# Optimization experiments

Hardware: AMD Instinct MI355X
Metric: run time of the kernel (lower is better)

Reference implementation:

```python
import jax, jax.numpy as jnp
import numpy as np

NUM_CLASSES = 91
COST_CLASS, COST_BBOX, COST_GIOU = 1.0, 5.0, 2.0
W_CE, W_BBOX, W_GIOU = 2.0, 2.5, 2.0
EOS_COEF = 0.1
B, Q, T = 64, 300, 25


def box_cxcywh_to_xyxy(x):
    cx, cy, w, h = x[..., 0], x[..., 1], x[..., 2], x[..., 3]
    return jnp.stack([cx - 0.5 * w, cy - 0.5 * h, cx + 0.5 * w, cy + 0.5 * h], axis=-1)


def giou_pairwise(b1, b2):
    # b1 [N,4], b2 [M,4] in xyxy -> [N,M]
    area1 = (b1[:, 2] - b1[:, 0]) * (b1[:, 3] - b1[:, 1])
    area2 = (b2[:, 2] - b2[:, 0]) * (b2[:, 3] - b2[:, 1])
    lt = jnp.maximum(b1[:, None, :2], b2[None, :, :2])
    rb = jnp.minimum(b1[:, None, 2:], b2[None, :, 2:])
    wh = jnp.clip(rb - lt, 0.0)
    inter = wh[..., 0] * wh[..., 1]
    union = area1[:, None] + area2[None, :] - inter
    iou = inter / union
    lti = jnp.minimum(b1[:, None, :2], b2[None, :, :2])
    rbi = jnp.maximum(b1[:, None, 2:], b2[None, :, 2:])
    whi = jnp.clip(rbi - lti, 0.0)
    areai = whi[..., 0] * whi[..., 1]
    return iou - (areai - union) / areai


def giou_elementwise(b1, b2):
    # b1,b2 [N,4] xyxy -> [N]
    area1 = (b1[:, 2] - b1[:, 0]) * (b1[:, 3] - b1[:, 1])
    area2 = (b2[:, 2] - b2[:, 0]) * (b2[:, 3] - b2[:, 1])
    lt = jnp.maximum(b1[:, :2], b2[:, :2])
    rb = jnp.minimum(b1[:, 2:], b2[:, 2:])
    wh = jnp.clip(rb - lt, 0.0)
    inter = wh[:, 0] * wh[:, 1]
    union = area1 + area2 - inter
    iou = inter / union
    lti = jnp.minimum(b1[:, :2], b2[:, :2])
    rbi = jnp.maximum(b1[:, 2:], b2[:, 2:])
    whi = jnp.clip(rbi - lti, 0.0)
    areai = whi[:, 0] * whi[:, 1]
    return iou - (areai - union) / areai


def _lsa(cost):
    # Jonker-Volgenant shortest augmenting path; same optimum as scipy linear_sum_assignment
    cost = np.asarray(cost, dtype=np.float64)
    transposed = cost.shape[0] > cost.shape[1]
    if transposed:
        cost = cost.T
    n, m = cost.shape  # n <= m
    u = np.zeros(n + 1)
    v = np.zeros(m + 1)
    p = np.zeros(m + 1, dtype=np.int64)
    way = np.zeros(m + 1, dtype=np.int64)
    for i in range(1, n + 1):
        p[0] = i
        j0 = 0
        minv = np.full(m + 1, np.inf)
        used = np.zeros(m + 1, dtype=bool)
        while True:
            used[j0] = True
            i0 = p[j0]
            cur = cost[i0 - 1, :] - u[i0] - v[1:]
            free = ~used[1:]
            better = free & (cur < minv[1:])
            minv[1:][better] = cur[better]
            way[1:][better] = j0
            masked = np.where(free, minv[1:], np.inf)
            j1 = int(np.argmin(masked)) + 1
            delta = minv[j1]
            u[p[used]] += delta
            v[used] -= delta
            minv[~used] -= delta
            j0 = j1
            if p[j0] == 0:
                break
        while j0:
            j1 = way[j0]
            p[j0] = p[j1]
            j0 = j1
    rows, cols = [], []
    for j in range(1, m + 1):
        if p[j] != 0:
            rows.append(p[j] - 1)
            cols.append(j - 1)
    rows = np.asarray(rows, dtype=np.int64)
    cols = np.asarray(cols, dtype=np.int64)
    if transposed:
        rows, cols = cols, rows
    order = np.argsort(rows)
    return rows[order], cols[order]


def _match(pred_logits, pred_boxes, tgt_labels, tgt_boxes):
    # builds the full cross-batch cost matrix exactly like the torch module, then
    # solves per-image rectangular assignment on the host (non-differentiable)
    log_prob = jax.nn.log_softmax(pred_logits.reshape(B * Q, NUM_CLASSES + 1), axis=-1)
    out_bbox = pred_boxes.reshape(B * Q, 4)
    tgt_ids = tgt_labels.reshape(B * T)
    tgt_bb = tgt_boxes.reshape(B * T, 4)
    cost_class = -log_prob[:, tgt_ids]                                        # [BQ, BT]
    cost_bbox = jnp.abs(out_bbox[:, None, :] - tgt_bb[None, :, :]).sum(-1)    # L1 cdist
    cost_giou = -giou_pairwise(box_cxcywh_to_xyxy(out_bbox), box_cxcywh_to_xyxy(tgt_bb))
    C = COST_BBOX * cost_bbox + COST_CLASS * cost_class + COST_GIOU * cost_giou
    Cn = np.asarray(jax.lax.stop_gradient(C.reshape(B, Q, B * T)))
    src = np.zeros((B, T), dtype=np.int64)
    tgt = np.zeros((B, T), dtype=np.int64)
    for b in range(B):
        r, c = _lsa(Cn[b, :, b * T:(b + 1) * T])
        src[b] = r
        tgt[b] = c
    batch_idx = jnp.repeat(jnp.arange(B), T)
    return batch_idx, jnp.asarray(src.reshape(-1)), jnp.asarray(tgt.reshape(-1))


def _losses(pred_logits, pred_boxes, tgt_labels, tgt_boxes, batch_idx, src_idx, tgt_idx):
    num_t = batch_idx.shape[0]
    matched_labels = tgt_labels[batch_idx, tgt_idx]
    target_classes = jnp.full((B, Q), NUM_CLASSES, dtype=jnp.int32)
    target_classes = target_classes.at[batch_idx, src_idx].set(matched_labels)
    empty_weight = jnp.ones(NUM_CLASSES + 1, dtype=pred_logits.dtype).at[-1].set(EOS_COEF)
    logp = jax.nn.log_softmax(pred_logits, axis=-1)
    nll = -jnp.take_along_axis(logp, target_classes[..., None], axis=-1)[..., 0]
    w = empty_weight[target_classes]
    loss_ce = (w * nll).sum() / w.sum()
    src_b = pred_boxes[batch_idx, src_idx]
    tgt_b = tgt_boxes[batch_idx, tgt_idx]
    loss_bbox = jnp.abs(src_b - tgt_b).sum() / num_t
    loss_giou = (1.0 - giou_elementwise(box_cxcywh_to_xyxy(src_b), box_cxcywh_to_xyxy(tgt_b))).sum() / num_t
    l_ce = W_CE * loss_ce
    l_bb = W_BBOX * loss_bbox
    l_gi = W_GIOU * loss_giou
    return jnp.stack([l_ce, l_bb, l_gi, l_ce + l_bb + l_gi])


def setup_inputs() -> dict:
    key = jax.random.key(0)
    k1, k2, k3, k4 = jax.random.split(key, 4)
    pred_logits = jax.random.normal(k1, (B, Q, NUM_CLASSES + 1), dtype=jnp.float32)
    pred_boxes = jax.random.uniform(k2, (B, Q, 4), dtype=jnp.float32, minval=0.05, maxval=0.95)
    tgt_labels = jax.random.randint(k3, (B, T), 0, NUM_CLASSES)
    tgt_boxes = jax.random.uniform(k4, (B, T, 4), dtype=jnp.float32, minval=0.05, maxval=0.95)
    return {"pred_logits": pred_logits, "pred_boxes": pred_boxes, "tgt_labels": tgt_labels, "tgt_boxes": tgt_boxes}


def reference(pred_logits, pred_boxes, tgt_labels, tgt_boxes):
    batch_idx, src_idx, tgt_idx = _match(pred_logits, pred_boxes, tgt_labels, tgt_boxes)
    # returns [loss_ce, loss_bbox, loss_giou, loss_total] (already weight-scaled)
    return _losses(pred_logits, pred_boxes, tgt_labels, tgt_boxes, batch_idx, src_idx, tgt_idx)
```

## Files before the change

kernel.cpp:

```cpp
#include <hip/hip_runtime.h>
#include <math.h>

constexpr int B_ = 64;
constexpr int Q_ = 300;
constexpr int T_ = 25;
constexpr int NCLS = 91;
constexpr int L_ = NCLS + 1;
constexpr float C_BB = 5.0f, C_GI = 2.0f;
constexpr float W_CE = 2.0f, W_BBOX = 2.5f, W_GIOU = 2.0f;
constexpr float EOS = 0.1f;
constexpr int K_ = 5;
constexpr int TPB = 256;

__device__ __forceinline__ unsigned long long ord64(double v) {
    long long bb = __double_as_longlong(v);
    return (bb < 0) ? ~(unsigned long long)bb
                    : ((unsigned long long)bb | 0x8000000000000000ULL);
}
__device__ __forceinline__ double unord64(unsigned long long u) {
    long long bb = (u & 0x8000000000000000ULL) ? (long long)(u & 0x7FFFFFFFFFFFFFFFULL)
                                               : (long long)~u;
    return __longlong_as_double(bb);
}
__device__ __forceinline__ unsigned long long pack14(double v, unsigned aux) {
    return (ord64(v) & ~16383ULL) | (unsigned long long)aux;
}
__device__ __forceinline__ unsigned long long pack9(double v, unsigned col) {
    return (ord64(v) & ~511ULL) | (unsigned long long)col;
}

template <int CTRL>
__device__ __forceinline__ unsigned long long dppb(unsigned long long b) {
    int lo = __builtin_amdgcn_update_dpp(0, (int)(unsigned)b, CTRL, 0xF, 0xF, true);
    int hi = __builtin_amdgcn_update_dpp(0, (int)(unsigned)(b >> 32), CTRL, 0xF, 0xF, true);
    return ((unsigned long long)(unsigned)hi << 32) | (unsigned)lo;
}
__device__ __forceinline__ unsigned long long swz16(unsigned long long b) {
    int lo = __builtin_amdgcn_ds_swizzle((int)(unsigned)b, 0x401F);
    int hi = __builtin_amdgcn_ds_swizzle((int)(unsigned)(b >> 32), 0x401F);
    return ((unsigned long long)(unsigned)hi << 32) | (unsigned)lo;
}

__device__ __forceinline__ unsigned long long wavemin(unsigned long long b) {
    { unsigned long long o = __shfl_xor(b, 32); if (o < b) b = o; }
    { unsigned long long o = swz16(b);      if (o < b) b = o; }
    { unsigned long long o = dppb<0x140>(b); if (o < b) b = o; }
    { unsigned long long o = dppb<0x141>(b); if (o < b) b = o; }
    { unsigned long long o = dppb<0x4E>(b);  if (o < b) b = o; }
    { unsigned long long o = dppb<0xB1>(b);  if (o < b) b = o; }
    return b;
}
__device__ __forceinline__ void red2(unsigned long long& k1, unsigned long long& k2,
                                     unsigned long long o1, unsigned long long o2) {
    unsigned long long n1 = o1 < k1 ? o1 : k1;
    unsigned long long ls = o1 < k1 ? k1 : o1;
    unsigned long long n2 = k2 < o2 ? k2 : o2;
    n2 = ls < n2 ? ls : n2;
    k1 = n1; k2 = n2;
}
__device__ __forceinline__ void wavemin2(unsigned long long& k1, unsigned long long& k2) {
    red2(k1, k2, __shfl_xor(k1, 32), __shfl_xor(k2, 32));
    red2(k1, k2, swz16(k1), swz16(k2));
    red2(k1, k2, dppb<0x140>(k1), dppb<0x140>(k2));
    red2(k1, k2, dppb<0x141>(k1), dppb<0x141>(k2));
    red2(k1, k2, dppb<0x4E>(k1),  dppb<0x4E>(k2));
    red2(k1, k2, dppb<0xB1>(k1),  dppb<0xB1>(k2));
}

__device__ __forceinline__ float giou_f(const float px[4], float parea,
                                        const float tx[4], float tarea) {
    float ltx = fmaxf(px[0], tx[0]), lty = fmaxf(px[1], tx[1]);
    float rbx = fminf(px[2], tx[2]), rby = fminf(px[3], tx[3]);
    float iw = fmaxf(rbx - ltx, 0.f), ih = fmaxf(rby - lty, 0.f);
    float inter = iw * ih;
    float uni = parea + tarea - inter;
    float iou = inter / uni;
    float lix = fminf(px[0], tx[0]), liy = fminf(px[1], tx[1]);
    float rix = fmaxf(px[2], tx[2]), riy = fmaxf(px[3], tx[3]);
    float aw = fmaxf(rix - lix, 0.f), ah = fmaxf(riy - liy, 0.f);
    float ai = aw * ah;
    return iou - (ai - uni) / ai;
}

__global__ __launch_bounds__(TPB) void fused_kernel(
        const float* __restrict__ logits,
        const float* __restrict__ pboxes,
        const int*   __restrict__ tlabels,
        const float* __restrict__ tboxes,
        double* __restrict__ partial) {
    const int b = blockIdx.x;
    const int tid = threadIdx.x;

    __shared__ float  costL[T_][Q_];
    __shared__ float  lseL[Q_];
    __shared__ int    pL[Q_ + 1];
    __shared__ int    wayL[Q_ + 1];
    __shared__ double uStage[32];
    __shared__ int    argcolL[T_];
    __shared__ float  m1L[T_];
    __shared__ double m2L[T_];
    __shared__ int    mqL[T_];
    __shared__ int    lblL[T_];
    __shared__ int    lblq[Q_];
    __shared__ float  tbL[T_][4];
    __shared__ float  txL[T_][4];
    __shared__ float  taL[T_];
    __shared__ double wsum[4][3];

    if (tid < T_) {
        lblL[tid] = tlabels[b * T_ + tid];
        mqL[tid] = 0;
        float c0 = tboxes[(size_t)(b * T_ + tid) * 4 + 0];
        float c1 = tboxes[(size_t)(b * T_ + tid) * 4 + 1];
        float c2 = tboxes[(size_t)(b * T_ + tid) * 4 + 2];
        float c3 = tboxes[(size_t)(b * T_ + tid) * 4 + 3];
        tbL[tid][0] = c0; tbL[tid][1] = c1; tbL[tid][2] = c2; tbL[tid][3] = c3;
        float x0 = c0 - 0.5f * c2, y0 = c1 - 0.5f * c3;
        float x1 = c0 + 0.5f * c2, y1 = c1 + 0.5f * c3;
        txL[tid][0] = x0; txL[tid][1] = y0; txL[tid][2] = x1; txL[tid][3] = y1;
        taL[tid] = (x1 - x0) * (y1 - y0);
    }
    for (int j = tid; j <= Q_; j += TPB) { pL[j] = 0; wayL[j] = 0; }
    for (int q = tid; q < Q_; q += TPB) lblq[q] = NCLS;
    __syncthreads();

    const float* lgb = logits + (size_t)b * Q_ * L_;
    const float* pbb = pboxes + (size_t)b * Q_ * 4;

    for (int q = tid; q < Q_; q += TPB) {
        const float4* lr4 = (const float4*)(lgb + (size_t)q * L_);
        float m0 = -INFINITY, m1 = -INFINITY, m2 = -INFINITY, m3 = -INFINITY;
        for (int c = 0; c < 23; ++c) {
            float4 v = lr4[c];
            m0 = fmaxf(m0, v.x); m1 = fmaxf(m1, v.y);
            m2 = fmaxf(m2, v.z); m3 = fmaxf(m3, v.w);
        }
        float mx = fmaxf(fmaxf(m0, m1), fmaxf(m2, m3));
        float s0 = 0.f, s1 = 0.f, s2 = 0.f, s3 = 0.f;
        for (int c = 0; c < 23; ++c) {
            float4 v = lr4[c];
            s0 += expf(v.x - mx); s1 += expf(v.y - mx);
            s2 += expf(v.z - mx); s3 += expf(v.w - mx);
        }
        float lz = mx + logf((s0 + s1) + (s2 + s3));
        lseL[q] = lz;

        float p0 = pbb[(size_t)q * 4 + 0], p1 = pbb[(size_t)q * 4 + 1];
        float p2 = pbb[(size_t)q * 4 + 2], p3 = pbb[(size_t)q * 4 + 3];
        float px[4] = { p0 - 0.5f * p2, p1 - 0.5f * p3, p0 + 0.5f * p2, p1 + 0.5f * p3 };
        float parea = (px[2] - px[0]) * (px[3] - px[1]);

#pragma unroll
        for (int t = 0; t < T_; ++t) {
            float cls = lz - lgb[(size_t)q * L_ + lblL[t]];
            float l1 = fabsf(p0 - tbL[t][0]) + fabsf(p1 - tbL[t][1]) +
                       fabsf(p2 - tbL[t][2]) + fabsf(p3 - tbL[t][3]);
            float tx[4] = { txL[t][0], txL[t][1], txL[t][2], txL[t][3] };
            float g = giou_f(px, parea, tx, taL[t]);
            costL[t][q] = C_BB * l1 + cls - C_GI * g;
        }
    }
    __syncthreads();

    {
        int w = tid >> 6, lane = tid & 63;
        for (int t = w; t < T_; t += 4) {
            unsigned long long k1 = ~0ULL, k2 = ~0ULL;
#pragma unroll
            for (int k = 0; k < K_; ++k) {
                int col = lane + 64 * k;
                if (col < Q_) {
                    unsigned long long kk = pack9((double)costL[t][col], (unsigned)col);
                    if (kk < k1) { k2 = k1; k1 = kk; }
                    else if (kk < k2) { k2 = kk; }
                }
            }
            wavemin2(k1, k2);
            if (lane == 0) {
                int jc = (int)(k1 & 511ULL);
                argcolL[t] = jc;
                m1L[t] = costL[t][jc];
                m2L[t] = unord64(k2 & ~511ULL);
            }
        }
    }
    __syncthreads();

    if (tid < 64) {
        bool isrow = (tid >= 1 && tid <= T_);
        int r0 = tid - 1;
        int myc = isrow ? argcolL[r0] : -1;
        bool winner = isrow;
        if (isrow) {
            for (int j = 0; j < r0; ++j)
                if (argcolL[j] == myc) winner = false;
        }
        int rowcol = (isrow && winner) ? myc + 1 : 0;
        unsigned long long mbal = __ballot(isrow && winner);
        unsigned int freemask = (~(unsigned int)(mbal >> 1)) & ((1u << T_) - 1);

        double ureg = 0.0;
        if (isrow) ureg = winner ? m2L[r0] : (double)m1L[r0];

        double v0[K_], minv[K_], stampv[K_];
        int pReg[K_];
        bool usedk[K_], validk[K_];
#pragma unroll
        for (int k = 0; k < K_; ++k) {
            int col = tid + 64 * k;
            validk[k] = col < Q_;
            v0[k] = 0.0; stampv[k] = 0.0; usedk[k] = false; minv[k] = INFINITY;
            pReg[k] = 0;
        }

        for (int t = 0; t < T_; ++t) {
            if ((mbal >> (t + 1)) & 1ULL) {
                int jc = argcolL[t];
                if (tid == (jc & 63)) {
                    int ki = jc >> 6;
                    double d = m2L[t] - (double)m1L[t];
                    if (d < 0.0) d = 0.0;
#pragma unroll
                    for (int k = 0; k < K_; ++k)
                        if (k == ki) { v0[k] -= d; pReg[k] = t + 1; }
                }
            }
        }

        for (int iter = 0; iter < 96 && freemask; ++iter) {
            int t = __builtin_ctz(freemask);
            freemask &= freemask - 1;
            const float* crow = &costL[t][0];
            unsigned long long k1 = ~0ULL, k2 = ~0ULL;
#pragma unroll
            for (int k = 0; k < K_; ++k) {
                if (validk[k]) {
                    int col = tid + 64 * k;
                    unsigned long long kk = pack9((double)crow[col] - v0[k], (unsigned)col);
                    if (kk < k1) { k2 = k1; k1 = kk; }
                    else if (kk < k2) { k2 = kk; }
                }
            }
            wavemin2(k1, k2);
            int j1 = (int)(k1 & 511ULL);
            double am1 = unord64(k1 & ~511ULL);
            double am2 = unord64(k2 & ~511ULL);
            unsigned long long bal = __ballot(rowcol == j1 + 1);
            int prev1 = bal ? __builtin_ctzll(bal) : 0;
            if (tid == (j1 & 63)) {
                int ki = j1 >> 6;
#pragma unroll
                for (int k = 0; k < K_; ++k)
                    if (k == ki) { v0[k] -= (am2 - am1); pReg[k] = t + 1; }
            }
            if (tid == t + 1) { ureg = am2; rowcol = j1 + 1; }
            if (prev1) {
                if (tid == prev1) rowcol = 0;
                freemask |= 1u << (prev1 - 1);
            }
        }

#pragma unroll
        for (int k = 0; k < K_; ++k)
            if (validk[k]) pL[tid + 1 + 64 * k] = pReg[k];

        for (int i = 1; i <= T_; ++i) {
            if (!((freemask >> (i - 1)) & 1u)) continue;
            if (tid == 0) pL[0] = i;
#pragma unroll
            for (int k = 0; k < K_; ++k) { minv[k] = INFINITY; usedk[k] = false; }
            double S = 0.0;
            int j0 = 0, i0 = i;
            double u0i0 = __shfl(ureg, i);

            for (int step = 0; step < 512; ++step) {
                double a = u0i0 - S;
                const float* crow = &costL[i0 - 1][0];
                unsigned long long bk = ~0ULL;
#pragma unroll
                for (int k = 0; k < K_; ++k) {
                    if (validk[k] && !usedk[k]) {
                        int col = tid + 64 * k;
                        double cur = (double)crow[col] - a - v0[k];
                        if (cur < minv[k]) { minv[k] = cur; wayL[col + 1] = j0; }
                        unsigned long long kk = pack14(
                            minv[k], ((unsigned)(col + 1) << 5) | (unsigned)pReg[k]);
                        if (kk < bk) bk = kk;
                    }
                }
                bk = wavemin(bk);
                int j1  = (int)((bk >> 5) & 511ULL);
                int i0n = (int)(bk & 31ULL);
                double Snew = unord64(bk & ~16383ULL);
                S = Snew;
                j0 = j1;
                if (i0n == 0) break;
                int owner = (j1 - 1) & 63, k1i = (j1 - 1) >> 6;
                if (tid == owner) {
#pragma unroll
                    for (int k = 0; k < K_; ++k)
                        if (k == k1i) { usedk[k] = true; stampv[k] = Snew; }
                }
                i0 = i0n;
                u0i0 = __shfl(ureg, i0);
            }

            if (tid <= T_) uStage[tid] = 0.0;
#pragma unroll
            for (int k = 0; k < K_; ++k) {
                if (validk[k] && usedk[k]) {
                    double d = S - stampv[k];
                    v0[k] -= d;
                    uStage[pReg[k]] = d;
                }
            }
            if (tid >= 1 && tid <= T_) ureg += uStage[tid];
            if (tid == i) ureg += S;
            if (tid == 0) {
                int jj = j0;
                while (jj) { int jn = wayL[jj]; pL[jj] = pL[jn]; jj = jn; }
            }
#pragma unroll
            for (int k = 0; k < K_; ++k)
                if (validk[k]) pReg[k] = pL[tid + 1 + 64 * k];
        }

#pragma unroll
        for (int k = 0; k < K_; ++k)
            if (validk[k] && pReg[k] > 0) mqL[pReg[k] - 1] = tid + 64 * k;
        if (tid < T_) lblq[mqL[tid]] = lblL[tid];
    }
    __syncthreads();

    double ce = 0.0, sb = 0.0, sg = 0.0;
    for (int q = tid; q < Q_; q += TPB) {
        int label = lblq[q];
        float nll = lseL[q] - lgb[(size_t)q * L_ + label];
        float w = (label == NCLS) ? EOS : 1.0f;
        ce += (double)(w * nll);
    }
    if (tid < T_) {
        int q = mqL[tid];
        float p0 = pbb[(size_t)q * 4 + 0], p1 = pbb[(size_t)q * 4 + 1];
        float p2 = pbb[(size_t)q * 4 + 2], p3 = pbb[(size_t)q * 4 + 3];
        sb = (double)(fabsf(p0 - tbL[tid][0]) + fabsf(p1 - tbL[tid][1]) +
                      fabsf(p2 - tbL[tid][2]) + fabsf(p3 - tbL[tid][3]));
        float px[4] = { p0 - 0.5f * p2, p1 - 0.5f * p3, p0 + 0.5f * p2, p1 + 0.5f * p3 };
        float parea = (px[2] - px[0]) * (px[3] - px[1]);
        float tx[4] = { txL[tid][0], txL[tid][1], txL[tid][2], txL[tid][3] };
        float g = giou_f(px, parea, tx, taL[tid]);
        sg = (double)(1.0f - g);
    }
#pragma unroll
    for (int off = 1; off < 64; off <<= 1) {
        ce += __shfl_xor(ce, off);
        sb += __shfl_xor(sb, off);
        sg += __shfl_xor(sg, off);
    }
    if ((tid & 63) == 0) {
        int w = tid >> 6;
        wsum[w][0] = ce; wsum[w][1] = sb; wsum[w][2] = sg;
    }
    __syncthreads();
    if (tid == 0) {
        double a0 = 0, a1 = 0, a2 = 0;
        for (int w = 0; w < 4; ++w) { a0 += wsum[w][0]; a1 += wsum[w][1]; a2 += wsum[w][2]; }
        partial[(size_t)b * 3 + 0] = a0;
        partial[(size_t)b * 3 + 1] = a1;
        partial[(size_t)b * 3 + 2] = a2;
    }
}

__global__ __launch_bounds__(64) void finalize_kernel(const double* __restrict__ partial,
                                                      float* __restrict__ out) {
    int tid = threadIdx.x;
    double a = partial[(size_t)tid * 3 + 0];
    double c = partial[(size_t)tid * 3 + 1];
    double g = partial[(size_t)tid * 3 + 2];
#pragma unroll
    for (int off = 1; off < 64; off <<= 1) {
        a += __shfl_xor(a, off);
        c += __shfl_xor(c, off);
        g += __shfl_xor(g, off);
    }
    if (tid == 0) {
        float lce = W_CE * (float)(a / 3360.0);
        float lbb = W_BBOX * (float)(c / 1600.0);
        float lgi = W_GIOU * (float)(g / 1600.0);
        out[0] = lce;
        out[1] = lbb;
        out[2] = lgi;
        out[3] = lce + lbb + lgi;
    }
}

extern "C" void kernel_launch(void* const* d_in, const int* in_sizes, int n_in,
                              void* d_out, int out_size, void* d_ws, size_t ws_size,
                              hipStream_t stream) {
    (void)in_sizes; (void)n_in; (void)out_size; (void)ws_size;
    const float* logits  = (const float*)d_in[0];
    const float* pboxes  = (const float*)d_in[1];
    const int*   tlabels = (const int*)d_in[2];
    const float* tboxes  = (const float*)d_in[3];
    float* out = (float*)d_out;
    double* partial = (double*)d_ws;

    fused_kernel<<<B_, TPB, 0, stream>>>(logits, pboxes, tlabels, tboxes, partial);
    finalize_kernel<<<1, 64, 0, stream>>>(partial, out);
}
```

Baseline: 39.99 us.

## Parallelize auction-style augmentation across four waves and fuse finalize via atomics

The single-wave serial augmentation phase becomes a multi-wave round loop. Each of the 4 waves bids for a different free row, and thread 0 resolves column conflicts and updates prices held in shared memory (vL, uL). The dual variables move from registers to shared memory so every wave can see them. The separate finalize kernel is removed: blocks accumulate with double atomics, and the last block, found with a counter, writes the output. A memset is added to zero the accumulator. The change trades per-round __syncthreads and serial resolution for fewer serial iterations, and it removes a kernel launch.

New measurement: 41.90 us. 1.05x slower.

```diff
diff --git a/kernel.cpp b/kernel.cpp
--- a/kernel.cpp
+++ b/kernel.cpp
@@ -87,18 +87,24 @@
         const float* __restrict__ pboxes,
         const int*   __restrict__ tlabels,
         const float* __restrict__ tboxes,
-        double* __restrict__ partial) {
+        double* acc,
+        float* out) {
     const int b = blockIdx.x;
     const int tid = threadIdx.x;
 
     __shared__ float  costL[T_][Q_];
     __shared__ float  lseL[Q_];
+    __shared__ double vL[Q_];
     __shared__ int    pL[Q_ + 1];
     __shared__ int    wayL[Q_ + 1];
-    __shared__ double uStage[32];
+    __shared__ double uL[T_ + 1];
     __shared__ int    argcolL[T_];
     __shared__ float  m1L[T_];
     __shared__ double m2L[T_];
+    __shared__ int    bidRowL[4];
+    __shared__ int    bidJL[4];
+    __shared__ double bidM1L[4], bidM2L[4];
+    __shared__ unsigned freemaskL;
     __shared__ int    mqL[T_];
     __shared__ int    lblL[T_];
     __shared__ int    lblq[Q_];
@@ -121,7 +127,7 @@
         taL[tid] = (x1 - x0) * (y1 - y0);
     }
     for (int j = tid; j <= Q_; j += TPB) { pL[j] = 0; wayL[j] = 0; }
-    for (int q = tid; q < Q_; q += TPB) lblq[q] = NCLS;
+    for (int q = tid; q < Q_; q += TPB) { lblq[q] = NCLS; vL[q] = 0.0; }
     __syncthreads();
 
     const float* lgb = logits + (size_t)b * Q_ * L_;
@@ -195,13 +201,76 @@
             for (int j = 0; j < r0; ++j)
                 if (argcolL[j] == myc) winner = false;
         }
-        int rowcol = (isrow && winner) ? myc + 1 : 0;
+        if (isrow) {
+            uL[tid] = winner ? m2L[r0] : (double)m1L[r0];
+            if (winner) {
+                pL[myc + 1] = tid;
+                double d = m2L[r0] - (double)m1L[r0];
+                if (d < 0.0) d = 0.0;
+                vL[myc] = -d;
+            }
+        }
         unsigned long long mbal = __ballot(isrow && winner);
-        unsigned int freemask = (~(unsigned int)(mbal >> 1)) & ((1u << T_) - 1);
-
-        double ureg = 0.0;
-        if (isrow) ureg = winner ? m2L[r0] : (double)m1L[r0];
-
+        if (tid == 0) freemaskL = (~(unsigned)(mbal >> 1)) & ((1u << T_) - 1);
+    }
+
+    for (int round = 0; round < 40; ++round) {
+        __syncthreads();
+        unsigned fm = freemaskL;
+        if (!fm) break;
+        int w = tid >> 6, lane = tid & 63;
+        unsigned m = fm;
+        for (int i = 0; i < w; ++i) m &= m - 1;
+        int myrow = m ? (int)__builtin_ctz(m) : -1;
+        unsigned long long k1 = ~0ULL, k2 = ~0ULL;
+        if (myrow >= 0) {
+            const float* crow = &costL[myrow][0];
+#pragma unroll
+            for (int k = 0; k < K_; ++k) {
+                int col = lane + 64 * k;
+                if (col < Q_) {
+                    double cur = (double)crow[col] - vL[col];
+                    unsigned long long kk = pack9(cur, (unsigned)col);
+                    if (kk < k1) { k2 = k1; k1 = kk; }
+                    else if (kk < k2) { k2 = kk; }
+                }
+            }
+            wavemin2(k1, k2);
+        }
+        if (lane == 0) {
+            bidRowL[w] = myrow;
+            if (myrow >= 0) {
+                bidJL[w]  = (int)(k1 & 511ULL);
+                bidM1L[w] = unord64(k1 & ~511ULL);
+                bidM2L[w] = unord64(k2 & ~511ULL);
+            }
+        }
+        __syncthreads();
+        if (tid == 0) {
+            int c0 = -1, c1 = -1, c2 = -1;
+            unsigned f2 = fm;
+            for (int ww = 0; ww < 4; ++ww) {
+                int r = bidRowL[ww];
+                if (r < 0) continue;
+                int j = bidJL[ww];
+                if (j == c0 || j == c1 || j == c2) continue;
+                if (c0 < 0) c0 = j; else if (c1 < 0) c1 = j; else c2 = j;
+                double d = bidM2L[ww] - bidM1L[ww];
+                if (d < 0.0) d = 0.0;
+                int prev = pL[j + 1];
+                pL[j + 1] = r + 1;
+                uL[r + 1] = bidM2L[ww];
+                vL[j] -= d;
+                f2 &= ~(1u << r);
+                if (prev) f2 |= 1u << (prev - 1);
+            }
+            freemaskL = f2;
+        }
+    }
+    __syncthreads();
+
+    if (tid < 64) {
+        unsigned freemask = freemaskL;
         double v0[K_], minv[K_], stampv[K_];
         int pReg[K_];
         bool usedk[K_], validk[K_];
@@ -209,60 +278,10 @@
         for (int k = 0; k < K_; ++k) {
             int col = tid + 64 * k;
             validk[k] = col < Q_;
-            v0[k] = 0.0; stampv[k] = 0.0; usedk[k] = false; minv[k] = INFINITY;
-            pReg[k] = 0;
-        }
-
-        for (int t = 0; t < T_; ++t) {
-            if ((mbal >> (t + 1)) & 1ULL) {
-                int jc = argcolL[t];
-                if (tid == (jc & 63)) {
-                    int ki = jc >> 6;
-                    double d = m2L[t] - (double)m1L[t];
-                    if (d < 0.0) d = 0.0;
-#pragma unroll
-                    for (int k = 0; k < K_; ++k)
-                        if (k == ki) { v0[k] -= d; pReg[k] = t + 1; }
-                }
-            }
-        }
-
-        for (int iter = 0; iter < 96 && freemask; ++iter) {
-            int t = __builtin_ctz(freemask);
-            freemask &= freemask - 1;
-            const float* crow = &costL[t][0];
-            unsigned long long k1 = ~0ULL, k2 = ~0ULL;
-#pragma unroll
-            for (int k = 0; k < K_; ++k) {
-                if (validk[k]) {
-                    int col = tid + 64 * k;
-                    unsigned long long kk = pack9((double)crow[col] - v0[k], (unsigned)col);
-                    if (kk < k1) { k2 = k1; k1 = kk; }
-                    else if (kk < k2) { k2 = kk; }
-                }
-            }
-            wavemin2(k1, k2);
-            int j1 = (int)(k1 & 511ULL);
-            double am1 = unord64(k1 & ~511ULL);
-            double am2 = unord64(k2 & ~511ULL);
-            unsigned long long bal = __ballot(rowcol == j1 + 1);
-            int prev1 = bal ? __builtin_ctzll(bal) : 0;
-            if (tid == (j1 & 63)) {
-                int ki = j1 >> 6;
-#pragma unroll
-                for (int k = 0; k < K_; ++k)
-                    if (k == ki) { v0[k] -= (am2 - am1); pReg[k] = t + 1; }
-            }
-            if (tid == t + 1) { ureg = am2; rowcol = j1 + 1; }
-            if (prev1) {
-                if (tid == prev1) rowcol = 0;
-                freemask |= 1u << (prev1 - 1);
-            }
-        }
-
-#pragma unroll
-        for (int k = 0; k < K_; ++k)
-            if (validk[k]) pL[tid + 1 + 64 * k] = pReg[k];
+            v0[k] = validk[k] ? vL[col] : 0.0;
+            stampv[k] = 0.0; usedk[k] = false; minv[k] = INFINITY;
+            pReg[k] = validk[k] ? pL[col + 1] : 0;
+        }
 
         for (int i = 1; i <= T_; ++i) {
             if (!((freemask >> (i - 1)) & 1u)) continue;
@@ -271,7 +290,7 @@
             for (int k = 0; k < K_; ++k) { minv[k] = INFINITY; usedk[k] = false; }
             double S = 0.0;
             int j0 = 0, i0 = i;
-            double u0i0 = __shfl(ureg, i);
+            double u0i0 = uL[i];
 
             for (int step = 0; step < 512; ++step) {
                 double a = u0i0 - S;
@@ -302,21 +321,19 @@
                         if (k == k1i) { usedk[k] = true; stampv[k] = Snew; }
                 }
                 i0 = i0n;
-                u0i0 = __shfl(ureg, i0);
-            }
-
-            if (tid <= T_) uStage[tid] = 0.0;
+                u0i0 = uL[i0];
+            }
+
 #pragma unroll
             for (int k = 0; k < K_; ++k) {
                 if (validk[k] && usedk[k]) {
                     double d = S - stampv[k];
                     v0[k] -= d;
-                    uStage[pReg[k]] = d;
+                    uL[pReg[k]] += d;
                 }
             }
-            if (tid >= 1 && tid <= T_) ureg += uStage[tid];
-            if (tid == i) ureg += S;
             if (tid == 0) {
+                uL[i] += S;
                 int jj = j0;
                 while (jj) { int jn = wayL[jj]; pL[jj] = pL[jn]; jj = jn; }
             }
@@ -362,35 +379,29 @@
         wsum[w][0] = ce; wsum[w][1] = sb; wsum[w][2] = sg;
     }
     __syncthreads();
+
     if (tid == 0) {
         double a0 = 0, a1 = 0, a2 = 0;
         for (int w = 0; w < 4; ++w) { a0 += wsum[w][0]; a1 += wsum[w][1]; a2 += wsum[w][2]; }
-        partial[(size_t)b * 3 + 0] = a0;
-        partial[(size_t)b * 3 + 1] = a1;
-        partial[(size_t)b * 3 + 2] = a2;
-    }
-}
-
-__global__ __launch_bounds__(64) void finalize_kernel(const double* __restrict__ partial,
-                                                      float* __restrict__ out) {
-    int tid = threadIdx.x;
-    double a = partial[(size_t)tid * 3 + 0];
-    double c = partial[(size_t)tid * 3 + 1];
-    double g = partial[(size_t)tid * 3 + 2];
-#pragma unroll
-    for (int off = 1; off < 64; off <<= 1) {
-        a += __shfl_xor(a, off);
-        c += __shfl_xor(c, off);
-        g += __shfl_xor(g, off);
-    }
-    if (tid == 0) {
-        float lce = W_CE * (float)(a / 3360.0);
-        float lbb = W_BBOX * (float)(c / 1600.0);
-        float lgi = W_GIOU * (float)(g / 1600.0);
-        out[0] = lce;
-        out[1] = lbb;
-        out[2] = lgi;
-        out[3] = lce + lbb + lgi;
+        atomicAdd(&acc[0], a0);
+        atomicAdd(&acc[1], a1);
+        atomicAdd(&acc[2], a2);
+        __threadfence();
+        unsigned* cnt = (unsigned*)(acc + 3);
+        unsigned old = atomicAdd(cnt, 1u);
+        if (old == (unsigned)(B_ - 1)) {
+            __threadfence();
+            double A = atomicAdd(&acc[0], 0.0);
+            double C = atomicAdd(&acc[1], 0.0);
+            double G = atomicAdd(&acc[2], 0.0);
+            float lce = W_CE * (float)(A / 3360.0);
+            float lbb = W_BBOX * (float)(C / 1600.0);
+            float lgi = W_GIOU * (float)(G / 1600.0);
+            out[0] = lce;
+            out[1] = lbb;
+            out[2] = lgi;
+            out[3] = lce + lbb + lgi;
+        }
     }
 }
 
@@ -403,8 +414,8 @@
     const int*   tlabels = (const int*)d_in[2];
     const float* tboxes  = (const float*)d_in[3];
     float* out = (float*)d_out;
-    double* partial = (double*)d_ws;
-
-    fused_kernel<<<B_, TPB, 0, stream>>>(logits, pboxes, tlabels, tboxes, partial);
-    finalize_kernel<<<1, 64, 0, stream>>>(partial, out);
-}
+    double* acc = (double*)d_ws;
+
+    hipMemsetAsync(d_ws, 0, 64, stream);
+    fused_kernel<<<B_, TPB, 0, stream>>>(logits, pboxes, tlabels, tboxes, acc, out);
+}
```
